# Kernel optimization log

Hardware: AMD Instinct MI355X
Metric: run time of the kernel (lower is better)

Reference implementation:

```python
import jax, jax.numpy as jnp
import numpy as np

B, T, C, NH = 8, 1024, 1024, 16
HD = C // NH
EPS = 1e-5


def setup_inputs() -> dict:
    key = jax.random.key(0)
    k1, k2, k3 = jax.random.split(key, 3)
    x = jax.random.normal(k1, (B, T, C), dtype=jnp.float32)
    past_kv = jax.random.normal(k2, (NH, HD, HD), dtype=jnp.float32) * 0.1
    W_qkv = jax.random.normal(k3, (C, 3 * C), dtype=jnp.float32) * 0.02
    gn_weight = jnp.ones((NH,), dtype=jnp.float32)
    gn_bias = jnp.zeros((NH,), dtype=jnp.float32)
    return {"x": x, "past_kv": past_kv, "W_qkv": W_qkv,
            "gn_weight": gn_weight, "gn_bias": gn_bias}


def _decay_mask(nh, t, dtype):
    # decay_mask[h, i, j] = gamma[h]**(i-j) if i >= j else 0
    gamma = 1.0 - 2.0 ** (-5.0 - jnp.arange(nh, dtype=jnp.float32))
    idx = jnp.arange(t)
    diff = idx[:, None] - idx[None, :]            # [T, T]
    mask = diff >= 0
    pow_ = gamma[:, None, None] ** jnp.where(mask, diff, 0).astype(jnp.float32)
    return jnp.where(mask[None], pow_, 0.0).astype(dtype), gamma.astype(dtype)


def reference(x, past_kv, W_qkv, gn_weight, gn_bias):
    b, t, c = x.shape
    nh = gn_weight.shape[0]
    hd = c // nh

    qkv = x @ W_qkv                               # [B, T, 3C]
    q, k, v = jnp.split(qkv, 3, axis=2)
    split_heads = lambda u: u.reshape(b, t, nh, hd).transpose(0, 2, 1, 3)  # [B,nh,T,hd]
    q, k, v = split_heads(q), split_heads(k), split_heads(v)

    decay, gamma = _decay_mask(nh, t, x.dtype)    # [nh,T,T], [nh]

    # intra-chunk: decay-masked QK^T @ V
    ret = jnp.einsum('bhtd,bhsd->bhts', q, k) * decay      # [B,nh,T,T]
    inner = jnp.einsum('bhts,bhsd->bhtd', ret, v)          # [B,nh,T,hd]

    # cross-chunk: q @ past_kv * (n_head * chunk_size)
    inner_decay = float(nh * hd)
    cross = jnp.einsum('bhtd,hde->bhte', q, past_kv) * inner_decay
    r = inner + cross                                      # [B,nh,T,hd]

    # recurrent state update: gamma * past_kv + k^T @ v, then mean over batch
    current_kv = gamma[:, None, None] * past_kv + jnp.einsum('bhtd,bhte->bhde', k, v)
    current_kv = current_kv.mean(axis=0)                   # [nh,hd,hd]

    # GroupNorm(1, n_head) on [B, nh, hd, T] (single group => stats over all non-batch dims)
    y = r.transpose(0, 1, 3, 2)                            # [B,nh,hd,T]
    mu = y.mean(axis=(1, 2, 3), keepdims=True)
    var = y.var(axis=(1, 2, 3), keepdims=True)             # biased, matches torch GroupNorm
    yn = (y - mu) * jax.lax.rsqrt(var + EPS)
    yn = yn * gn_weight[None, :, None, None] + gn_bias[None, :, None, None]

    # rearrange 'b c h t -> b t (c h)'
    out = yn.transpose(0, 3, 1, 2).reshape(b, t, c)
    return out, current_kv
```

## Files before the change

### kernel.cpp

```cpp
#include <hip/hip_runtime.h>


#define TKN 8192
#define N3  3072

typedef short short8 __attribute__((ext_vector_type(8)));
typedef float f32x4 __attribute__((ext_vector_type(4)));

static __device__ __forceinline__ unsigned short f2bf(float f){
  unsigned int u = __float_as_uint(f);
  u += 0x7FFFu + ((u >> 16) & 1u);
  return (unsigned short)(u >> 16);
}
static __device__ __forceinline__ float bf2f(unsigned short s){
  return __uint_as_float(((unsigned int)s) << 16);
}
static __device__ __forceinline__ void g2lds16(const void* g, void* l){
  __builtin_amdgcn_global_load_lds(
      (const __attribute__((address_space(1))) unsigned int*)g,
      (__attribute__((address_space(3))) unsigned int*)l, 16, 0, 0);
}

__global__ __launch_bounds__(256) void k_cvt(const float* __restrict__ x,
                                             const float* __restrict__ w,
                                             const float* __restrict__ pk,
                                             unsigned short* __restrict__ xb,
                                             unsigned short* __restrict__ wt,
                                             unsigned short* __restrict__ pkt){
  __shared__ float tile[64][65];
  const int bid = blockIdx.x;
  if (bid < 2048){
    const int n4 = TKN*1024/4;
    for (int idx = bid*256 + threadIdx.x; idx < n4; idx += 2048*256){
      float4 v = reinterpret_cast<const float4*>(x)[idx];
      ushort4 o;
      o.x = f2bf(v.x); o.y = f2bf(v.y); o.z = f2bf(v.z); o.w = f2bf(v.w);
      reinterpret_cast<ushort4*>(xb)[idx] = o;
    }
  } else if (bid < 2816){
    const int b2 = bid - 2048;
    const int n0 = (b2 % 48)*64, k0 = (b2 / 48)*64;
    const int tn = threadIdx.x & 63, t4 = threadIdx.x >> 6;
    for (int kk = t4; kk < 64; kk += 4)
      tile[kk][tn] = w[(k0+kk)*N3 + n0 + tn];
    __syncthreads();
    for (int nn = t4; nn < 64; nn += 4)
      wt[(n0+nn)*1024 + k0 + tn] = f2bf(tile[tn][nn]);
  } else {
    int i = (bid - 2816)*256 + threadIdx.x;
    int h = i >> 12, e = (i >> 6) & 63, d = i & 63;
    pkt[i] = f2bf(pk[(h<<12) + (d<<6) + e] * 1024.0f);
  }
}

__global__ __launch_bounds__(256, 3) void k_gemm(const unsigned short* __restrict__ A,
                                                 const unsigned short* __restrict__ Bt,
                                                 unsigned short* __restrict__ qb,
                                                 unsigned short* __restrict__ kb,
                                                 unsigned short* __restrict__ vtb){
  __shared__ unsigned short sm[24576];
  char* smb = (char*)sm;
  const int tid = threadIdx.x;
  const int lane = tid & 63, wid = tid >> 6;
  const int wm = wid >> 1, wn = wid & 1;
  const int n15 = lane & 15, l4 = lane >> 4;
  const int id = blockIdx.x;
  const int lin = (id & 7)*192 + (id >> 3);
  const int bm = lin / 24, bn = lin % 24;
  const int m0 = bm * 128;
  const int n0 = bn * 128;

  f32x4 acc[4][4] = {};

  const int l0 = tid >> 2;
  const int r0 = (l0 & ~3) | ((l0 & 1) << 1) | ((l0 >> 1) & 1);
  const int c0 = (((tid & 3) ^ ((tid >> 4) & 3)) << 3);
  #define STAGE(kt, b) do {                                                              \
    g2lds16(A  + (long)(m0 + r0)*1024      + (kt)*32 + c0, smb + (b)*8192 + tid*16);     \
    g2lds16(A  + (long)(m0 + 64 + r0)*1024 + (kt)*32 + c0, smb + (b)*8192 + 4096 + tid*16); \
    g2lds16(Bt + (long)(n0 + r0)*1024      + (kt)*32 + c0, smb + 24576 + (b)*8192 + tid*16); \
    g2lds16(Bt + (long)(n0 + 64 + r0)*1024 + (kt)*32 + c0, smb + 24576 + (b)*8192 + 4096 + tid*16); \
  } while(0)

  STAGE(0, 0);
  STAGE(1, 1);
  asm volatile("s_waitcnt vmcnt(4)" ::: "memory");
  __builtin_amdgcn_s_barrier();

  const int slb = (l4 ^ ((n15 >> 2) & 3)) << 4;
  int cur = 0;
  for (int t = 0; t < 32; ++t){
    int nb = cur + 2; if (nb >= 3) nb -= 3;
    if (t < 30) STAGE(t + 2, nb);
    const char* ab = smb + cur*8192;
    const char* bb = smb + 24576 + cur*8192;
    short8 a[4], b[4];
    #pragma unroll
    for (int i = 0; i < 4; ++i){
      int ra = wm*64 + i*16 + n15;
      int rs = (ra & ~3) | ((ra & 1) << 1) | ((ra >> 1) & 1);
      a[i] = *(const short8*)(ab + rs*64 + slb);
      int rb = wn*64 + i*16 + n15;
      int rbs = (rb & ~3) | ((rb & 1) << 1) | ((rb >> 1) & 1);
      b[i] = *(const short8*)(bb + rbs*64 + slb);
    }
    __builtin_amdgcn_s_setprio(1);
    #pragma unroll
    for (int i = 0; i < 4; ++i)
      #pragma unroll
      for (int j = 0; j < 4; ++j)
        acc[i][j] = __builtin_amdgcn_mfma_f32_16x16x32_bf16(a[i], b[j], acc[i][j], 0, 0, 0);
    __builtin_amdgcn_s_setprio(0);
    if (t < 30) asm volatile("s_waitcnt vmcnt(4)" ::: "memory");
    else        asm volatile("s_waitcnt vmcnt(0)" ::: "memory");
    __builtin_amdgcn_s_barrier();
    cur = cur + 1; if (cur == 3) cur = 0;
  }
  #undef STAGE

  const int bb2 = m0 >> 10;
  const int which = n0 >> 10;
  const int cw = (n0 & 1023) + wn*64;
  const int h = cw >> 6;
  const long bh = (long)(bb2*16 + h);
  const int trow0 = (m0 & 1023) + wm*64;
  char* W = smb + wid*8192;

  if (which < 2){
    unsigned short* dst = which ? kb : qb;
    #pragma unroll
    for (int mi = 0; mi < 4; ++mi)
      #pragma unroll
      for (int nf = 0; nf < 4; ++nf)
        #pragma unroll
        for (int r = 0; r < 4; ++r){
          int row = mi*16 + l4*4 + r;
          int colb = (nf*32 + 2*n15) ^ ((row & 7) << 4);
          *(unsigned short*)(W + row*128 + colb) = f2bf(acc[mi][nf][r]);
        }
    asm volatile("s_waitcnt lgkmcnt(0)" ::: "memory");
    #pragma unroll
    for (int hh = 0; hh < 2; ++hh)
      #pragma unroll
      for (int c2 = 0; c2 < 4; ++c2){
        int row = hh*32 + (lane >> 1);
        int off = ((lane & 1)*64 + c2*16) ^ ((row & 7) << 4);
        uint4 v = *(const uint4*)(W + row*128 + off);
        int dcol = (lane & 1)*32 + c2*8;
        *(uint4*)(&dst[(bh*1024 + trow0 + row)*64 + dcol]) = v;
      }
  } else {
    #pragma unroll
    for (int mi = 0; mi < 4; ++mi)
      #pragma unroll
      for (int nf = 0; nf < 4; ++nf)
        #pragma unroll
        for (int r = 0; r < 4; ++r){
          int dl = nf*16 + n15;
          int row = mi*16 + l4*4 + r;
          int colb = (2*row) ^ ((dl & 7) << 4);
          *(unsigned short*)(W + dl*128 + colb) = f2bf(acc[mi][nf][r]);
        }
    asm volatile("s_waitcnt lgkmcnt(0)" ::: "memory");
    #pragma unroll
    for (int hh = 0; hh < 2; ++hh)
      #pragma unroll
      for (int c2 = 0; c2 < 4; ++c2){
        int dl = hh*32 + (lane >> 1);
        int off = ((lane & 1)*64 + c2*16) ^ ((dl & 7) << 4);
        uint4 v = *(const uint4*)(W + dl*128 + off);
        int tcol = (lane & 1)*32 + c2*8;
        *(uint4*)(&vtb[(bh*64 + dl)*1024 + trow0 + tcol]) = v;
      }
  }
}

__global__ __launch_bounds__(256) void k_attn(const unsigned short* __restrict__ qb,
                                              const unsigned short* __restrict__ kb,
                                              const unsigned short* __restrict__ vtb,
                                              const unsigned short* __restrict__ pkt,
                                              unsigned short* __restrict__ rb,
                                              float* __restrict__ gnp){
  __shared__ unsigned short Qs[8192];
  __shared__ unsigned short Kd[2][4096];
  __shared__ unsigned short Vd[2][4096];
  __shared__ unsigned short Ps[8192];
  __shared__ float gred[2][4];
  const int id = blockIdx.x;
  const int lin = (id & 7)*64 + (id >> 3);
  const int qpair = lin & 3;
  const int bh = lin >> 2;
  const int h = bh & 15;
  const int tid = threadIdx.x;
  const int lane = tid & 63, wid = tid >> 6;
  const int n15 = lane & 15, l4 = lane >> 4;
  const unsigned short* qp = qb + (long)bh*65536;
  const unsigned short* kp = kb + (long)bh*65536;
  const unsigned short* vp = vtb + (long)bh*65536;
  const float lg = log2f(1.0f - exp2f(-5.0f - (float)h));
  const int srow = tid >> 3, schunk = tid & 7;

  float kvE[4][4];
  #pragma unroll
  for (int i = 0; i < 4; ++i)
    #pragma unroll
    for (int r = 0; r < 4; ++r)
      kvE[i][r] = exp2f(-lg * (float)(i*16 + l4*4 + r));

  float gs = 0.f, gq = 0.f;
  unsigned short* rp = rb + (long)bh*65536;

  for (int p = 0; p < 2; ++p){
    const int qt = p ? (7 - qpair) : qpair;
    const int t0 = qt * 128;
    for (int c = 0; c < 4; ++c){
      int r = c*32 + srow;
      int src = schunk ^ (r & 7);
      g2lds16(qp + (long)(t0 + r)*64 + src*8, (char*)Qs + c*4096 + tid*16);
    }
    for (int c = 0; c < 2; ++c){
      int r = c*32 + srow;
      int src = schunk ^ (r & 7);
      g2lds16(pkt + (long)(h*64 + r)*64 + src*8, (char*)Ps + c*4096 + tid*16);
      g2lds16(kp + (long)r*64 + src*8, (char*)Kd[0] + c*4096 + tid*16);
      g2lds16(vp + (long)r*1024 + src*8, (char*)Vd[0] + c*4096 + tid*16);
    }
    asm volatile("s_waitcnt vmcnt(0)" ::: "memory");
    __syncthreads();

    short8 aq[2][2];
    #pragma unroll
    for (int mf = 0; mf < 2; ++mf)
      #pragma unroll
      for (int kk = 0; kk < 2; ++kk){
        int r = wid*32 + mf*16 + n15;
        int sl = (kk*4 + l4) ^ (r & 7);
        aq[mf][kk] = *reinterpret_cast<const short8*>((const char*)Qs + r*128 + sl*16);
      }

    f32x4 o[2][4] = {};
    #pragma unroll
    for (int kk = 0; kk < 2; ++kk){
      short8 bpk[4];
      #pragma unroll
      for (int nf = 0; nf < 4; ++nf){
        int r = nf*16 + n15;
        int sl = (kk*4 + l4) ^ (r & 7);
        bpk[nf] = *reinterpret_cast<const short8*>((const char*)Ps + r*128 + sl*16);
      }
      #pragma unroll
      for (int mf = 0; mf < 2; ++mf)
        #pragma unroll
        for (int nf = 0; nf < 4; ++nf)
          o[mf][nf] = __builtin_amdgcn_mfma_f32_16x16x32_bf16(aq[mf][kk], bpk[nf], o[mf][nf], 0,0,0);
    }
    __syncthreads();

    const int jmax = 2*qt + 1;
    int cur = 0;
    for (int j = 0; j <= jmax; ++j){
      const int kv0 = j*64;
      if (j < jmax){
        const int kvn = kv0 + 64;
        for (int c = 0; c < 2; ++c){
          int r = c*32 + srow;
          int src = schunk ^ (r & 7);
          g2lds16(kp + (long)(kvn + r)*64 + src*8, (char*)Kd[cur^1] + c*4096 + tid*16);
          g2lds16(vp + (long)r*1024 + kvn + src*8, (char*)Vd[cur^1] + c*4096 + tid*16);
        }
      }
      const bool active = (kv0 <= t0 + wid*32 + 31);
      if (active){
        f32x4 sT[4][2] = {};
        #pragma unroll
        for (int kk = 0; kk < 2; ++kk){
          short8 bk[4];
          #pragma unroll
          for (int i = 0; i < 4; ++i){
            int r = i*16 + n15;
            int sl = (kk*4 + l4) ^ (r & 7);
            bk[i] = *reinterpret_cast<const short8*>((const char*)Kd[cur] + r*128 + sl*16);
          }
          #pragma unroll
          for (int i = 0; i < 4; ++i)
            #pragma unroll
            for (int mf = 0; mf < 2; ++mf)
              sT[i][mf] = __builtin_amdgcn_mfma_f32_16x16x32_bf16(bk[i], aq[mf][kk], sT[i][mf], 0,0,0);
        }
        const bool diag = (kv0 + 63 > t0 + wid*32);
        #pragma unroll
        for (int mf = 0; mf < 2; ++mf){
          const int trow = wid*32 + mf*16 + n15;
          const float rowE = exp2f(lg * (float)(t0 + trow - kv0));
          char* wb = (char*)Ps + trow*128;
          const int swz = (trow & 7) << 4;
          #pragma unroll
          for (int i = 0; i < 4; ++i){
            float v0 = sT[i][mf][0] * (rowE * kvE[i][0]);
            float v1 = sT[i][mf][1] * (rowE * kvE[i][1]);
            float v2 = sT[i][mf][2] * (rowE * kvE[i][2]);
            float v3 = sT[i][mf][3] * (rowE * kvE[i][3]);
            if (diag){
              int dd = (t0 + trow) - (kv0 + i*16 + l4*4);
              if (dd < 0) v0 = 0.f;
              if (dd < 1) v1 = 0.f;
              if (dd < 2) v2 = 0.f;
              if (dd < 3) v3 = 0.f;
            }
            uint2 pw;
            pw.x = (unsigned int)f2bf(v0) | ((unsigned int)f2bf(v1) << 16);
            pw.y = (unsigned int)f2bf(v2) | ((unsigned int)f2bf(v3) << 16);
            *(uint2*)(wb + ((i*32 + l4*8) ^ swz)) = pw;
          }
        }
        #pragma unroll
        for (int kk = 0; kk < 2; ++kk){
          short8 ap[2], bv[4];
          #pragma unroll
          for (int mf = 0; mf < 2; ++mf){
            int r = wid*32 + mf*16 + n15;
            int sl = (kk*4 + l4) ^ (r & 7);
            ap[mf] = *reinterpret_cast<const short8*>((const char*)Ps + r*128 + sl*16);
          }
          #pragma unroll
          for (int nf = 0; nf < 4; ++nf){
            int r = nf*16 + n15;
            int sl = (kk*4 + l4) ^ (r & 7);
            bv[nf] = *reinterpret_cast<const short8*>((const char*)Vd[cur] + r*128 + sl*16);
          }
          #pragma unroll
          for (int mf = 0; mf < 2; ++mf)
            #pragma unroll
            for (int nf = 0; nf < 4; ++nf)
              o[mf][nf] = __builtin_amdgcn_mfma_f32_16x16x32_bf16(ap[mf], bv[nf], o[mf][nf], 0,0,0);
        }
      }
      asm volatile("s_waitcnt vmcnt(0)" ::: "memory");
      __syncthreads();
      cur ^= 1;
    }
    #pragma unroll
    for (int mf = 0; mf < 2; ++mf)
      #pragma unroll
      for (int nf = 0; nf < 4; ++nf)
        #pragma unroll
        for (int r = 0; r < 4; ++r){
          int trow = wid*32 + mf*16 + l4*4 + r;
          int d = nf*16 + n15;
          float v = o[mf][nf][r];
          gs += v; gq += v*v;
          *(unsigned short*)((char*)Ps + trow*128 + ((2*d) ^ ((trow & 7) << 4))) = f2bf(v);
        }
    asm volatile("s_waitcnt lgkmcnt(0)" ::: "memory");
    #pragma unroll
    for (int rr = 0; rr < 4; ++rr){
      int row = wid*32 + rr*8 + (lane >> 3);
      int off = (((lane & 7) << 4) ^ ((row & 7) << 4));
      uint4 v = *(const uint4*)((const char*)Ps + row*128 + off);
      *(uint4*)(rp + (long)(t0 + row)*64 + ((lane & 7) << 3)) = v;
    }
    __syncthreads();
  }
  #pragma unroll
  for (int off = 32; off > 0; off >>= 1){
    gs += __shfl_down(gs, off);
    gq += __shfl_down(gq, off);
  }
  if (lane == 0){ gred[0][wid] = gs; gred[1][wid] = gq; }
  __syncthreads();
  if (tid == 0){
    gnp[(bh*4 + qpair)*2]   = gred[0][0]+gred[0][1]+gred[0][2]+gred[0][3];
    gnp[(bh*4 + qpair)*2+1] = gred[1][0]+gred[1][1]+gred[1][2]+gred[1][3];
  }
}

__global__ __launch_bounds__(256) void k_kvpart(const unsigned short* __restrict__ kb,
                                                const unsigned short* __restrict__ vtb,
                                                float* __restrict__ part){
  __shared__ unsigned short Kt[64*64];
  __shared__ unsigned int   Vt32[64*33];
  const int id = blockIdx.x;
  const int lin = (id & 7)*64 + (id >> 3);
  const int tc = lin & 3, bh = lin >> 2;
  const int tid = threadIdx.x;
  const int d0 = (tid >> 4) << 2;
  const int e0 = (tid & 15) << 2;
  const unsigned short* kp = kb + (long)bh*65536;
  const unsigned short* vp = vtb + (long)bh*65536;
  float acc[4][4] = {{0.f}};
  for (int tt = 0; tt < 4; ++tt){
    const int tb = tc*256 + tt*64;
    __syncthreads();
    {
      int rr0 = tid >> 3, off = (tid & 7) * 8;
      for (int c = 0; c < 2; ++c){
        int r = c*32 + rr0;
        *reinterpret_cast<uint4*>(&Kt[r*64 + off]) =
            *reinterpret_cast<const uint4*>(&kp[(long)(tb + r)*64 + off]);
        uint4 vv = *reinterpret_cast<const uint4*>(&vp[(long)r*1024 + tb + off]);
        unsigned int* dv = &Vt32[r*33 + (off >> 1)];
        dv[0] = vv.x; dv[1] = vv.y; dv[2] = vv.z; dv[3] = vv.w;
      }
    }
    __syncthreads();
    const unsigned short* Vt = (const unsigned short*)Vt32;
    for (int t = 0; t < 64; ++t){
      float kv[4], vv[4];
      #pragma unroll
      for (int i = 0; i < 4; ++i) kv[i] = bf2f(Kt[t*64 + d0 + i]);
      #pragma unroll
      for (int i = 0; i < 4; ++i) vv[i] = bf2f(Vt[(e0 + i)*66 + t]);
      #pragma unroll
      for (int i = 0; i < 4; ++i)
        #pragma unroll
        for (int j = 0; j < 4; ++j) acc[i][j] += kv[i]*vv[j];
    }
  }
  float* pp = part + ((long)(tc*128 + bh) << 12);
  for (int i = 0; i < 4; ++i)
    for (int j = 0; j < 4; ++j)
      pp[(d0+i)*64 + e0 + j] = acc[i][j];
}

__global__ __launch_bounds__(256) void k_kvfin(const float* __restrict__ part,
                                               const float* __restrict__ pk,
                                               float* __restrict__ okv,
                                               const float* __restrict__ gnp,
                                               float* __restrict__ musig){
  if (blockIdx.x == 0 && threadIdx.x < 8){
    int b = threadIdx.x;
    float S = 0.f, Q = 0.f;
    for (int g = 0; g < 64; ++g){ S += gnp[b*128 + g*2]; Q += gnp[b*128 + g*2 + 1]; }
    float mu  = S * (1.0f/1048576.0f);
    float var = Q * (1.0f/1048576.0f) - mu*mu;
    musig[b*2]   = mu;
    musig[b*2+1] = rsqrtf(var + 1e-5f);
  }
  int i = blockIdx.x*256 + threadIdx.x;
  int h = i >> 12;
  float acc = 0.f;
  for (int tc = 0; tc < 4; ++tc)
    for (int b = 0; b < 8; ++b)
      acc += part[((long)(tc*128 + b*16 + h) << 12) + (i & 4095)];
  float gamma = 1.0f - exp2f(-5.0f - (float)h);
  okv[i] = gamma * pk[i] + acc * 0.125f;
}

__global__ __launch_bounds__(256) void k_gnnorm(const unsigned short* __restrict__ rbuf,
                                                const float* __restrict__ musig,
                                                const float* __restrict__ gw,
                                                const float* __restrict__ gb,
                                                float* __restrict__ out){
  const int n8 = TKN*1024/8;
  for (int idx = blockIdx.x*256 + threadIdx.x; idx < n8; idx += gridDim.x*256){
    int o = idx*8;
    int c = o & 1023;
    int t = (o >> 10) & 1023;
    int b = o >> 20;
    int h = c >> 6, d = c & 63;
    short8 v = *reinterpret_cast<const short8*>(rbuf + ((long)(b*16 + h) << 16) + t*64 + d);
    float rs = musig[b*2+1];
    float a = gw[h]*rs, b2 = gb[h] - musig[b*2]*a;
    float4 o0, o1;
    o0.x = bf2f((unsigned short)v[0])*a + b2;
    o0.y = bf2f((unsigned short)v[1])*a + b2;
    o0.z = bf2f((unsigned short)v[2])*a + b2;
    o0.w = bf2f((unsigned short)v[3])*a + b2;
    o1.x = bf2f((unsigned short)v[4])*a + b2;
    o1.y = bf2f((unsigned short)v[5])*a + b2;
    o1.z = bf2f((unsigned short)v[6])*a + b2;
    o1.w = bf2f((unsigned short)v[7])*a + b2;
    *reinterpret_cast<float4*>(out + o)     = o0;
    *reinterpret_cast<float4*>(out + o + 4) = o1;
  }
}

extern "C" void kernel_launch(void* const* d_in, const int* in_sizes, int n_in,
                              void* d_out, int out_size, void* d_ws, size_t ws_size,
                              hipStream_t stream){
  const float* x  = (const float*)d_in[0];
  const float* pk = (const float*)d_in[1];
  const float* w  = (const float*)d_in[2];
  const float* gw = (const float*)d_in[3];
  const float* gb = (const float*)d_in[4];
  float* out = (float*)d_out;
  char* ws = (char*)d_ws;

  unsigned short* Xb  = (unsigned short*)(ws);
  unsigned short* WTb = (unsigned short*)(ws + 16777216);
  unsigned short* Qb  = (unsigned short*)(ws + 23068672);
  unsigned short* Kb  = (unsigned short*)(ws + 39845888);
  unsigned short* VTb = (unsigned short*)(ws + 56623104);
  unsigned short* PKt = (unsigned short*)(ws + 73400320);
  unsigned short* Rb  = (unsigned short*)(ws + 73531392);
  float* KVp = (float*)(ws);
  float* GNp = (float*)(ws + 90308608);
  float* MuS = (float*)(ws + 90312704);

  k_cvt    <<<dim3(3072),    dim3(256), 0, stream>>>(x, w, pk, Xb, WTb, PKt);
  k_gemm   <<<dim3(1536),    dim3(256), 0, stream>>>(Xb, WTb, Qb, Kb, VTb);
  k_attn   <<<dim3(512),     dim3(256), 0, stream>>>(Qb, Kb, VTb, PKt, Rb, GNp);
  k_kvpart <<<dim3(512),     dim3(256), 0, stream>>>(Kb, VTb, KVp);
  k_kvfin  <<<dim3(256),     dim3(256), 0, stream>>>(KVp, pk, out + 8388608, GNp, MuS);
  k_gnnorm <<<dim3(1024),    dim3(256), 0, stream>>>(Rb, MuS, gw, gb, out);
}
```

Baseline: 161.0 us.

## Enlarge QKV GEMM tile to 256x128 with double-buffered LDS and 2D grid

Widens each QKV projection GEMM block from 128x128 to 256x128 output, so every B fragment feeds twice as many MFMAs and each block loads less data per flop. The LDS pipeline drops from three stages to two, waiting for all loads to finish every iteration. The grouped block-index swizzle is replaced by a plain 2D grid, and the occupancy hint in the launch bounds is removed. The epilogue writes the results in two 64-row halves through the same per-wave LDS scratch. In exchange it uses more accumulator registers, likely lowers occupancy, gives less overlap of loads with compute, and loses the L2-friendly block ordering.

```diff
diff --git a/kernel.cpp b/kernel.cpp
--- a/kernel.cpp
+++ b/kernel.cpp
@@ -53,68 +53,63 @@
   }
 }
 
-__global__ __launch_bounds__(256, 3) void k_gemm(const unsigned short* __restrict__ A,
-                                                 const unsigned short* __restrict__ Bt,
-                                                 unsigned short* __restrict__ qb,
-                                                 unsigned short* __restrict__ kb,
-                                                 unsigned short* __restrict__ vtb){
+__global__ __launch_bounds__(256) void k_gemm(const unsigned short* __restrict__ A,
+                                              const unsigned short* __restrict__ Bt,
+                                              unsigned short* __restrict__ qb,
+                                              unsigned short* __restrict__ kb,
+                                              unsigned short* __restrict__ vtb){
   __shared__ unsigned short sm[24576];
   char* smb = (char*)sm;
   const int tid = threadIdx.x;
   const int lane = tid & 63, wid = tid >> 6;
   const int wm = wid >> 1, wn = wid & 1;
   const int n15 = lane & 15, l4 = lane >> 4;
-  const int id = blockIdx.x;
-  const int lin = (id & 7)*192 + (id >> 3);
-  const int bm = lin / 24, bn = lin % 24;
-  const int m0 = bm * 128;
-  const int n0 = bn * 128;
-
-  f32x4 acc[4][4] = {};
+  const int n0 = blockIdx.x * 128;
+  const int m0 = blockIdx.y * 256;
+
+  f32x4 acc[8][4] = {};
 
   const int l0 = tid >> 2;
   const int r0 = (l0 & ~3) | ((l0 & 1) << 1) | ((l0 >> 1) & 1);
   const int c0 = (((tid & 3) ^ ((tid >> 4) & 3)) << 3);
-  #define STAGE(kt, b) do {                                                              \
-    g2lds16(A  + (long)(m0 + r0)*1024      + (kt)*32 + c0, smb + (b)*8192 + tid*16);     \
-    g2lds16(A  + (long)(m0 + 64 + r0)*1024 + (kt)*32 + c0, smb + (b)*8192 + 4096 + tid*16); \
-    g2lds16(Bt + (long)(n0 + r0)*1024      + (kt)*32 + c0, smb + 24576 + (b)*8192 + tid*16); \
-    g2lds16(Bt + (long)(n0 + 64 + r0)*1024 + (kt)*32 + c0, smb + 24576 + (b)*8192 + 4096 + tid*16); \
+  #define STAGE(kt, b) do {                                                                   \
+    g2lds16(A  + (long)(m0 + r0)*1024       + (kt)*32 + c0, smb + (b)*24576 + tid*16);        \
+    g2lds16(A  + (long)(m0 + 64 + r0)*1024  + (kt)*32 + c0, smb + (b)*24576 + 4096 + tid*16); \
+    g2lds16(A  + (long)(m0 + 128 + r0)*1024 + (kt)*32 + c0, smb + (b)*24576 + 8192 + tid*16); \
+    g2lds16(A  + (long)(m0 + 192 + r0)*1024 + (kt)*32 + c0, smb + (b)*24576 + 12288 + tid*16);\
+    g2lds16(Bt + (long)(n0 + r0)*1024       + (kt)*32 + c0, smb + (b)*24576 + 16384 + tid*16);\
+    g2lds16(Bt + (long)(n0 + 64 + r0)*1024  + (kt)*32 + c0, smb + (b)*24576 + 20480 + tid*16);\
   } while(0)
 
   STAGE(0, 0);
-  STAGE(1, 1);
-  asm volatile("s_waitcnt vmcnt(4)" ::: "memory");
+  asm volatile("s_waitcnt vmcnt(0)" ::: "memory");
   __builtin_amdgcn_s_barrier();
 
   const int slb = (l4 ^ ((n15 >> 2) & 3)) << 4;
-  int cur = 0;
   for (int t = 0; t < 32; ++t){
-    int nb = cur + 2; if (nb >= 3) nb -= 3;
-    if (t < 30) STAGE(t + 2, nb);
-    const char* ab = smb + cur*8192;
-    const char* bb = smb + 24576 + cur*8192;
-    short8 a[4], b[4];
-    #pragma unroll
-    for (int i = 0; i < 4; ++i){
-      int ra = wm*64 + i*16 + n15;
-      int rs = (ra & ~3) | ((ra & 1) << 1) | ((ra >> 1) & 1);
-      a[i] = *(const short8*)(ab + rs*64 + slb);
-      int rb = wn*64 + i*16 + n15;
+    if (t < 31) STAGE(t + 1, (t + 1) & 1);
+    const char* ab = smb + (t & 1)*24576;
+    const char* bb = ab + 16384;
+    short8 b[4];
+    #pragma unroll
+    for (int j = 0; j < 4; ++j){
+      int rb = wn*64 + j*16 + n15;
       int rbs = (rb & ~3) | ((rb & 1) << 1) | ((rb >> 1) & 1);
-      b[i] = *(const short8*)(bb + rbs*64 + slb);
+      b[j] = *(const short8*)(bb + rbs*64 + slb);
     }
     __builtin_amdgcn_s_setprio(1);
     #pragma unroll
-    for (int i = 0; i < 4; ++i)
+    for (int i = 0; i < 8; ++i){
+      int ra = wm*128 + i*16 + n15;
+      int ras = (ra & ~3) | ((ra & 1) << 1) | ((ra >> 1) & 1);
+      short8 a = *(const short8*)(ab + ras*64 + slb);
       #pragma unroll
       for (int j = 0; j < 4; ++j)
-        acc[i][j] = __builtin_amdgcn_mfma_f32_16x16x32_bf16(a[i], b[j], acc[i][j], 0, 0, 0);
+        acc[i][j] = __builtin_amdgcn_mfma_f32_16x16x32_bf16(a, b[j], acc[i][j], 0, 0, 0);
+    }
     __builtin_amdgcn_s_setprio(0);
-    if (t < 30) asm volatile("s_waitcnt vmcnt(4)" ::: "memory");
-    else        asm volatile("s_waitcnt vmcnt(0)" ::: "memory");
+    asm volatile("s_waitcnt vmcnt(0)" ::: "memory");
     __builtin_amdgcn_s_barrier();
-    cur = cur + 1; if (cur == 3) cur = 0;
   }
   #undef STAGE
 
@@ -123,55 +118,59 @@
   const int cw = (n0 & 1023) + wn*64;
   const int h = cw >> 6;
   const long bh = (long)(bb2*16 + h);
-  const int trow0 = (m0 & 1023) + wm*64;
+  const int t0w = (m0 & 1023) + wm*128;
   char* W = smb + wid*8192;
 
-  if (which < 2){
-    unsigned short* dst = which ? kb : qb;
-    #pragma unroll
-    for (int mi = 0; mi < 4; ++mi)
-      #pragma unroll
-      for (int nf = 0; nf < 4; ++nf)
-        #pragma unroll
-        for (int r = 0; r < 4; ++r){
-          int row = mi*16 + l4*4 + r;
-          int colb = (nf*32 + 2*n15) ^ ((row & 7) << 4);
-          *(unsigned short*)(W + row*128 + colb) = f2bf(acc[mi][nf][r]);
-        }
-    asm volatile("s_waitcnt lgkmcnt(0)" ::: "memory");
-    #pragma unroll
-    for (int hh = 0; hh < 2; ++hh)
-      #pragma unroll
-      for (int c2 = 0; c2 < 4; ++c2){
-        int row = hh*32 + (lane >> 1);
-        int off = ((lane & 1)*64 + c2*16) ^ ((row & 7) << 4);
-        uint4 v = *(const uint4*)(W + row*128 + off);
-        int dcol = (lane & 1)*32 + c2*8;
-        *(uint4*)(&dst[(bh*1024 + trow0 + row)*64 + dcol]) = v;
-      }
-  } else {
-    #pragma unroll
-    for (int mi = 0; mi < 4; ++mi)
-      #pragma unroll
-      for (int nf = 0; nf < 4; ++nf)
-        #pragma unroll
-        for (int r = 0; r < 4; ++r){
-          int dl = nf*16 + n15;
-          int row = mi*16 + l4*4 + r;
-          int colb = (2*row) ^ ((dl & 7) << 4);
-          *(unsigned short*)(W + dl*128 + colb) = f2bf(acc[mi][nf][r]);
-        }
-    asm volatile("s_waitcnt lgkmcnt(0)" ::: "memory");
-    #pragma unroll
-    for (int hh = 0; hh < 2; ++hh)
-      #pragma unroll
-      for (int c2 = 0; c2 < 4; ++c2){
-        int dl = hh*32 + (lane >> 1);
-        int off = ((lane & 1)*64 + c2*16) ^ ((dl & 7) << 4);
-        uint4 v = *(const uint4*)(W + dl*128 + off);
-        int tcol = (lane & 1)*32 + c2*8;
-        *(uint4*)(&vtb[(bh*64 + dl)*1024 + trow0 + tcol]) = v;
-      }
+  #pragma unroll
+  for (int hh2 = 0; hh2 < 2; ++hh2){
+    if (which < 2){
+      unsigned short* dst = which ? kb : qb;
+      #pragma unroll
+      for (int mi = 0; mi < 4; ++mi)
+        #pragma unroll
+        for (int nf = 0; nf < 4; ++nf)
+          #pragma unroll
+          for (int r = 0; r < 4; ++r){
+            int row = mi*16 + l4*4 + r;
+            int colb = (nf*32 + 2*n15) ^ ((row & 7) << 4);
+            *(unsigned short*)(W + row*128 + colb) = f2bf(acc[hh2*4 + mi][nf][r]);
+          }
+      asm volatile("s_waitcnt lgkmcnt(0)" ::: "memory");
+      #pragma unroll
+      for (int hh = 0; hh < 2; ++hh)
+        #pragma unroll
+        for (int c2 = 0; c2 < 4; ++c2){
+          int row = hh*32 + (lane >> 1);
+          int off = ((lane & 1)*64 + c2*16) ^ ((row & 7) << 4);
+          uint4 v = *(const uint4*)(W + row*128 + off);
+          int dcol = (lane & 1)*32 + c2*8;
+          *(uint4*)(&dst[(bh*1024 + t0w + hh2*64 + row)*64 + dcol]) = v;
+        }
+    } else {
+      #pragma unroll
+      for (int mi = 0; mi < 4; ++mi)
+        #pragma unroll
+        for (int nf = 0; nf < 4; ++nf)
+          #pragma unroll
+          for (int r = 0; r < 4; ++r){
+            int dl = nf*16 + n15;
+            int row = mi*16 + l4*4 + r;
+            int colb = (2*row) ^ ((dl & 7) << 4);
+            *(unsigned short*)(W + dl*128 + colb) = f2bf(acc[hh2*4 + mi][nf][r]);
+          }
+      asm volatile("s_waitcnt lgkmcnt(0)" ::: "memory");
+      #pragma unroll
+      for (int hh = 0; hh < 2; ++hh)
+        #pragma unroll
+        for (int c2 = 0; c2 < 4; ++c2){
+          int dl = hh*32 + (lane >> 1);
+          int off = ((lane & 1)*64 + c2*16) ^ ((dl & 7) << 4);
+          uint4 v = *(const uint4*)(W + dl*128 + off);
+          int tcol = (lane & 1)*32 + c2*8;
+          *(uint4*)(&vtb[(bh*64 + dl)*1024 + t0w + hh2*64 + tcol]) = v;
+        }
+    }
+    if (hh2 == 0){ asm volatile("s_waitcnt lgkmcnt(0)" ::: "memory"); }
   }
 }
 
@@ -498,7 +497,7 @@
   float* MuS = (float*)(ws + 90312704);
 
   k_cvt    <<<dim3(3072),    dim3(256), 0, stream>>>(x, w, pk, Xb, WTb, PKt);
-  k_gemm   <<<dim3(1536),    dim3(256), 0, stream>>>(Xb, WTb, Qb, Kb, VTb);
+  k_gemm   <<<dim3(24, 32),  dim3(256), 0, stream>>>(Xb, WTb, Qb, Kb, VTb);
   k_attn   <<<dim3(512),     dim3(256), 0, stream>>>(Qb, Kb, VTb, PKt, Rb, GNp);
   k_kvpart <<<dim3(512),     dim3(256), 0, stream>>>(Kb, VTb, KVp);
   k_kvfin  <<<dim3(256),     dim3(256), 0, stream>>>(KVp, pk, out + 8388608, GNp, MuS);
```

Result: slower. 185.0 us (+14.9%).

## Triple-buffer K/V prefetch in attention, reorder launches, simplify GEMM grid

Applied to the files above, without the earlier changes.

The attention loop now keeps two K/V tiles in flight by adding a third buffer that reuses the Q staging area once Q fragments are in registers. It waits with vmcnt(4) instead of draining all loads, which hides more global-load latency. The GEMM drops the XCD-aware linearized block remap in favour of a plain 2D grid, which may change L2 locality across chiplets. k_kvpart is also launched before k_attn; the two kernels are independent, so only the order changes.

```diff
diff --git a/kernel.cpp b/kernel.cpp
--- a/kernel.cpp
+++ b/kernel.cpp
@@ -64,11 +64,8 @@
   const int lane = tid & 63, wid = tid >> 6;
   const int wm = wid >> 1, wn = wid & 1;
   const int n15 = lane & 15, l4 = lane >> 4;
-  const int id = blockIdx.x;
-  const int lin = (id & 7)*192 + (id >> 3);
-  const int bm = lin / 24, bn = lin % 24;
-  const int m0 = bm * 128;
-  const int n0 = bn * 128;
+  const int m0 = blockIdx.y * 128;
+  const int n0 = blockIdx.x * 128;
 
   f32x4 acc[4][4] = {};
 
@@ -200,6 +197,9 @@
   const float lg = log2f(1.0f - exp2f(-5.0f - (float)h));
   const int srow = tid >> 3, schunk = tid & 7;
 
+  char* const kb0 = (char*)Kd[0]; char* const kb1 = (char*)Kd[1]; char* const kb2 = (char*)Qs;
+  char* const vb0 = (char*)Vd[0]; char* const vb1 = (char*)Vd[1]; char* const vb2 = (char*)Qs + 8192;
+
   float kvE[4][4];
   #pragma unroll
   for (int i = 0; i < 4; ++i)
@@ -213,6 +213,7 @@
   for (int p = 0; p < 2; ++p){
     const int qt = p ? (7 - qpair) : qpair;
     const int t0 = qt * 128;
+    const int jmax = 2*qt + 1;
     for (int c = 0; c < 4; ++c){
       int r = c*32 + srow;
       int src = schunk ^ (r & 7);
@@ -222,10 +223,16 @@
       int r = c*32 + srow;
       int src = schunk ^ (r & 7);
       g2lds16(pkt + (long)(h*64 + r)*64 + src*8, (char*)Ps + c*4096 + tid*16);
-      g2lds16(kp + (long)r*64 + src*8, (char*)Kd[0] + c*4096 + tid*16);
-      g2lds16(vp + (long)r*1024 + src*8, (char*)Vd[0] + c*4096 + tid*16);
-    }
-    asm volatile("s_waitcnt vmcnt(0)" ::: "memory");
+      g2lds16(kp + (long)r*64 + src*8, kb0 + c*4096 + tid*16);
+      g2lds16(vp + (long)r*1024 + src*8, vb0 + c*4096 + tid*16);
+    }
+    for (int c = 0; c < 2; ++c){
+      int r = c*32 + srow;
+      int src = schunk ^ (r & 7);
+      g2lds16(kp + (long)(64 + r)*64 + src*8, kb1 + c*4096 + tid*16);
+      g2lds16(vp + (long)r*1024 + 64 + src*8, vb1 + c*4096 + tid*16);
+    }
+    asm volatile("s_waitcnt vmcnt(4)" ::: "memory");
     __syncthreads();
 
     short8 aq[2][2];
@@ -256,21 +263,25 @@
     }
     __syncthreads();
 
-    const int jmax = 2*qt + 1;
-    int cur = 0;
+    int curb = 0, sjb = 2;
     for (int j = 0; j <= jmax; ++j){
       const int kv0 = j*64;
-      if (j < jmax){
-        const int kvn = kv0 + 64;
+      const bool willstage = (j + 2 <= jmax);
+      if (willstage){
+        const int kvn = kv0 + 128;
+        char* kbs = (sjb == 0) ? kb0 : ((sjb == 1) ? kb1 : kb2);
+        char* vbs = (sjb == 0) ? vb0 : ((sjb == 1) ? vb1 : vb2);
         for (int c = 0; c < 2; ++c){
           int r = c*32 + srow;
           int src = schunk ^ (r & 7);
-          g2lds16(kp + (long)(kvn + r)*64 + src*8, (char*)Kd[cur^1] + c*4096 + tid*16);
-          g2lds16(vp + (long)r*1024 + kvn + src*8, (char*)Vd[cur^1] + c*4096 + tid*16);
+          g2lds16(kp + (long)(kvn + r)*64 + src*8, kbs + c*4096 + tid*16);
+          g2lds16(vp + (long)r*1024 + kvn + src*8, vbs + c*4096 + tid*16);
         }
       }
       const bool active = (kv0 <= t0 + wid*32 + 31);
       if (active){
+        const char* kcur = (curb == 0) ? kb0 : ((curb == 1) ? kb1 : kb2);
+        const char* vcur = (curb == 0) ? vb0 : ((curb == 1) ? vb1 : vb2);
         f32x4 sT[4][2] = {};
         #pragma unroll
         for (int kk = 0; kk < 2; ++kk){
@@ -279,7 +290,7 @@
           for (int i = 0; i < 4; ++i){
             int r = i*16 + n15;
             int sl = (kk*4 + l4) ^ (r & 7);
-            bk[i] = *reinterpret_cast<const short8*>((const char*)Kd[cur] + r*128 + sl*16);
+            bk[i] = *reinterpret_cast<const short8*>(kcur + r*128 + sl*16);
           }
           #pragma unroll
           for (int i = 0; i < 4; ++i)
@@ -326,7 +337,7 @@
           for (int nf = 0; nf < 4; ++nf){
             int r = nf*16 + n15;
             int sl = (kk*4 + l4) ^ (r & 7);
-            bv[nf] = *reinterpret_cast<const short8*>((const char*)Vd[cur] + r*128 + sl*16);
+            bv[nf] = *reinterpret_cast<const short8*>(vcur + r*128 + sl*16);
           }
           #pragma unroll
           for (int mf = 0; mf < 2; ++mf)
@@ -335,9 +346,11 @@
               o[mf][nf] = __builtin_amdgcn_mfma_f32_16x16x32_bf16(ap[mf], bv[nf], o[mf][nf], 0,0,0);
         }
       }
-      asm volatile("s_waitcnt vmcnt(0)" ::: "memory");
+      if (willstage) asm volatile("s_waitcnt vmcnt(4)" ::: "memory");
+      else           asm volatile("s_waitcnt vmcnt(0)" ::: "memory");
       __syncthreads();
-      cur ^= 1;
+      curb = (curb == 2) ? 0 : curb + 1;
+      sjb  = (sjb  == 2) ? 0 : sjb  + 1;
     }
     #pragma unroll
     for (int mf = 0; mf < 2; ++mf)
@@ -498,9 +511,9 @@
   float* MuS = (float*)(ws + 90312704);
 
   k_cvt    <<<dim3(3072),    dim3(256), 0, stream>>>(x, w, pk, Xb, WTb, PKt);
-  k_gemm   <<<dim3(1536),    dim3(256), 0, stream>>>(Xb, WTb, Qb, Kb, VTb);
+  k_gemm   <<<dim3(24, 64),  dim3(256), 0, stream>>>(Xb, WTb, Qb, Kb, VTb);
+  k_kvpart <<<dim3(512),     dim3(256), 0, stream>>>(Kb, VTb, KVp);
   k_attn   <<<dim3(512),     dim3(256), 0, stream>>>(Qb, Kb, VTb, PKt, Rb, GNp);
-  k_kvpart <<<dim3(512),     dim3(256), 0, stream>>>(Kb, VTb, KVp);
   k_kvfin  <<<dim3(256),     dim3(256), 0, stream>>>(KVp, pk, out + 8388608, GNp, MuS);
   k_gnnorm <<<dim3(1024),    dim3(256), 0, stream>>>(Rb, MuS, gw, gb, out);
 }
```

Result: no change. 161.4 us (+0.2%).
